# Optimization experiments

Hardware: AMD Instinct MI355X
Metric: run time of the kernel (lower is better)

The kernel has to match this reference:

```python
import jax, jax.numpy as jnp
import numpy as np

B, N, F = 32, 1024, 7
HID, HID_GLO, MLP_H, OUT = 256, 8, 64, 8
THRESHOLD = 0.3


def setup_inputs() -> dict:
    key = jax.random.key(0)
    ks = jax.random.split(key, 16)
    def lin(k, fan_out, fan_in):
        # xavier-uniform-like init
        lim = (6.0 / (fan_in + fan_out)) ** 0.5
        return jax.random.uniform(k, (fan_out, fan_in), jnp.float32, -lim, lim)
    return {
        "x": jax.random.normal(ks[0], (B, N, F), jnp.float32),
        "W1": lin(ks[1], HID, 2),   "b1": jnp.zeros((HID,), jnp.float32),
        "W2": lin(ks[2], HID, HID), "b2": jnp.zeros((HID,), jnp.float32),
        "Wfc": lin(ks[3], HID, HID), "bfc": jnp.zeros((HID,), jnp.float32),
        "Wg": lin(ks[4], HID_GLO, 2), "bg": jnp.zeros((HID_GLO,), jnp.float32),
        "Wm0": lin(ks[5], MLP_H, N * F), "bm0": jnp.zeros((MLP_H,), jnp.float32),
        "Wm1": lin(ks[6], MLP_H, MLP_H), "bm1": jnp.zeros((MLP_H,), jnp.float32),
        "Wp": lin(ks[7], OUT, MLP_H + HID + HID_GLO), "bp": jnp.zeros((OUT,), jnp.float32),
    }


def reference(x, W1, b1, W2, b2, Wfc, bfc, Wg, bg, Wm0, bm0, Wm1, bm1, Wp, bp):
    # --- GCN branch (torch code detaches node features & adjacency) ---
    pts = jax.lax.stop_gradient(x[:, :, 1:3])                     # [B,N,2]
    diff = pts[:, :, None, :] - pts[:, None, :, :]                # [B,N,N,2]
    dist = jnp.sqrt(jnp.sum(diff * diff, axis=-1))                # [B,N,N]
    adj = (dist < THRESHOLD).astype(x.dtype)                      # [B,N,N]
    dinv = 1.0 / jnp.sqrt(jnp.sum(adj, axis=-1))                  # [B,N] (>=1, self-loop)
    nadj = dinv[:, :, None] * adj * dinv[:, None, :]              # D^-1/2 A D^-1/2
    h = jax.nn.relu(jnp.einsum('bij,bjd->bid', nadj, pts) @ W1.T + b1)   # [B,N,256]
    g = jnp.einsum('bij,bjh->bih', nadj, h) @ W2.T + b2                  # [B,N,256]
    gcn_en = jnp.mean(g, axis=1) @ Wfc.T + bfc                    # [B,256]

    # --- global branch (torch code uses .item() -> constants) ---
    v = jax.lax.stop_gradient(x[:, :, 1:5])                       # [B,N,4]
    avg_speed = jnp.mean(jnp.linalg.norm(v[:, :, 2:4], axis=-1), axis=1)  # [B]
    density = 1.0 / jnp.max(dist, axis=(1, 2))                    # [B] (v3 == pts)
    glo_in = jnp.stack([avg_speed, density], axis=-1)             # [B,2]
    glo_en = jax.nn.relu(glo_in @ Wg.T + bg)                      # [B,8]

    # --- MLP branch on flattened x ---
    xf = x.reshape(x.shape[0], -1)                                # [B, N*F]
    xf = jax.nn.relu(xf @ Wm0.T + bm0)
    xf = jax.nn.relu(xf @ Wm1.T + bm1)                            # [B,64]

    out = jnp.concatenate([xf, gcn_en, glo_en], axis=1) @ Wp.T + bp  # [B,8]
    return out
```

## Files before the change

### kernel.cpp

```cpp
#include <hip/hip_runtime.h>

#define BB 32
#define NN 1024
#define FF 7
#define HID 256
#define MLPH 64
#define OUTN 8
#define CATN (MLPH + HID + 8)

__device__ __forceinline__ float wave_sum(float v) {
#pragma unroll
    for (int m = 32; m >= 1; m >>= 1) v += __shfl_xor(v, m, 64);
    return v;
}
__device__ __forceinline__ float wave_max(float v) {
#pragma unroll
    for (int m = 32; m >= 1; m >>= 1) v = fmaxf(v, __shfl_xor(v, m, 64));
    return v;
}

__global__ __launch_bounds__(256) void kA(const float* __restrict__ x,
                                          const float* __restrict__ Wm0,
                                          const float* __restrict__ bm0,
                                          const float* __restrict__ W2,
                                          const float* __restrict__ b2,
                                          const float* __restrict__ Wfc,
                                          const float* __restrict__ bfc,
                                          const float* __restrict__ Wp,
                                          float* __restrict__ degp,
                                          float* __restrict__ bmax,
                                          float* __restrict__ sumsp,
                                          float* __restrict__ xf1,
                                          float* __restrict__ E,
                                          float* __restrict__ cE) {
    __shared__ __align__(16) float l0[256];
    __shared__ __align__(16) float l1[256];
    __shared__ float red[256];
    __shared__ float wred[4];
    int tid  = threadIdx.x;
    int lane = tid & 63;
    int w    = tid >> 6;
    if (blockIdx.x < 2048) {
        int blk = blockIdx.x;
        int b  = blk >> 6;
        int jg = (blk >> 2) & 15;
        int ks = blk & 3;
        const float* xb = x + b * (NN * FF);
        int n = ks * 256 + tid;
        l0[tid] = xb[n * FF + 1];
        l1[tid] = xb[n * FF + 2];
        int j = jg * 64 + lane;
        float pj0 = xb[j * FF + 1];
        float pj1 = xb[j * FF + 2];
        __syncthreads();
        const float4* v0p = (const float4*)&l0[w * 64];
        const float4* v1p = (const float4*)&l1[w * 64];
        unsigned degv = 0u;
        float mx = 0.f;
#pragma unroll 4
        for (int g = 0; g < 16; ++g) {
            float4 v0 = v0p[g], v1 = v1p[g];
            float dxa = pj0 - v0.x, dya = pj1 - v1.x;
            float dxb = pj0 - v0.y, dyb = pj1 - v1.y;
            float dxc = pj0 - v0.z, dyc = pj1 - v1.z;
            float dxd = pj0 - v0.w, dyd = pj1 - v1.w;
            float da = fmaf(dya, dya, dxa * dxa);
            float db = fmaf(dyb, dyb, dxb * dxb);
            float dc = fmaf(dyc, dyc, dxc * dxc);
            float dd = fmaf(dyd, dyd, dxd * dxd);
            degv += (da <= 0.09f);
            degv += (db <= 0.09f);
            degv += (dc <= 0.09f);
            degv += (dd <= 0.09f);
            mx = fmaxf(fmaxf(mx, fmaxf(da, db)), fmaxf(dc, dd));
        }
        red[tid] = (float)degv;
        __syncthreads();
        if (tid < 64) {
            degp[ks * (BB * NN) + b * NN + jg * 64 + tid] =
                red[tid] + red[tid + 64] + red[tid + 128] + red[tid + 192];
        }
        mx = wave_max(mx);
        if (lane == 0) wred[w] = mx;
        __syncthreads();
        if (tid == 0)
            bmax[b * 64 + jg * 4 + ks] =
                fmaxf(fmaxf(wred[0], wred[1]), fmaxf(wred[2], wred[3]));
        if (jg == 0 && ks == 0) {
            float sp = 0.f;
            for (int nn = tid; nn < NN; nn += 256) {
                float vx = xb[nn * FF + 3], vy = xb[nn * FF + 4];
                sp += sqrtf(vx * vx + vy * vy);
            }
            sp = wave_sum(sp);
            __syncthreads();
            if (lane == 0) wred[w] = sp;
            __syncthreads();
            if (tid == 0) sumsp[b] = wred[0] + wred[1] + wred[2] + wred[3];
        }
    } else if (blockIdx.x < 2560) {
        int blk = blockIdx.x - 2048;
        int b  = blk >> 4;
        int hq = blk & 15;
        int h = hq * 4 + w;
        const float4* wrow = (const float4*)(Wm0 + h * (NN * FF));
        const float4* xrow = (const float4*)(x + b * (NN * FF));
        float4 a4 = {0.f, 0.f, 0.f, 0.f};
#pragma unroll 7
        for (int it = 0; it < 28; ++it) {
            float4 wv = wrow[it * 64 + lane];
            float4 xv = xrow[it * 64 + lane];
            a4.x = fmaf(wv.x, xv.x, a4.x);
            a4.y = fmaf(wv.y, xv.y, a4.y);
            a4.z = fmaf(wv.z, xv.z, a4.z);
            a4.w = fmaf(wv.w, xv.w, a4.w);
        }
        float s = (a4.x + a4.y) + (a4.z + a4.w);
        s = wave_sum(s);
        if (lane == 0) xf1[b * MLPH + h] = fmaxf(s + bm0[h], 0.f);
    } else {
        int o = blockIdx.x - 2560;
        l0[tid] = Wp[o * CATN + MLPH + tid];
        __syncthreads();
        float a = 0.f;
#pragma unroll 8
        for (int m = 0; m < HID; ++m) a = fmaf(l0[m], Wfc[m * HID + tid], a);
        l1[tid] = a;
        red[tid] = l0[tid] * bfc[tid];
        __syncthreads();
        float e = 0.f;
#pragma unroll 8
        for (int k = 0; k < HID; ++k) e = fmaf(l1[k], W2[k * HID + tid], e);
        E[o * HID + tid] = e;
        float c = fmaf(l1[tid], b2[tid], red[tid]);
        c = wave_sum(c);
        if (lane == 0) wred[w] = c;
        __syncthreads();
        if (tid == 0) cE[o] = wred[0] + wred[1] + wred[2] + wred[3];
    }
}

__global__ __launch_bounds__(256) void kB(const float* __restrict__ x,
                                          const float* __restrict__ degp,
                                          float* __restrict__ q0p,
                                          float* __restrict__ q1p,
                                          float* __restrict__ wjp) {
    __shared__ __align__(16) float l0[256];
    __shared__ __align__(16) float l1[256];
    __shared__ __align__(16) float di[256];
    __shared__ float r0[256], r1[256], r2[256];
    int blk = blockIdx.x;
    int b  = blk >> 6;
    int jg = (blk >> 2) & 15;
    int ks = blk & 3;
    int tid  = threadIdx.x;
    int lane = tid & 63;
    int w    = tid >> 6;
    const float* xb = x + b * (NN * FF);
    int n = ks * 256 + tid;
    l0[tid] = xb[n * FF + 1];
    l1[tid] = xb[n * FF + 2];
    {
        int o = b * NN + n;
        float d = degp[o] + degp[BB * NN + o] + degp[2 * BB * NN + o] + degp[3 * BB * NN + o];
        di[tid] = 1.0f / sqrtf(d);
    }
    int j = jg * 64 + lane;
    float pj0 = xb[j * FF + 1];
    float pj1 = xb[j * FF + 2];
    __syncthreads();
    const float4* v0p = (const float4*)&l0[w * 64];
    const float4* v1p = (const float4*)&l1[w * 64];
    const float4* vdp = (const float4*)&di[w * 64];
    float a0 = 0.f, a1 = 0.f, as = 0.f;
#pragma unroll 4
    for (int g = 0; g < 16; ++g) {
        float4 v0 = v0p[g], v1 = v1p[g], vd = vdp[g];
        float dxa = pj0 - v0.x, dya = pj1 - v1.x;
        float dxb = pj0 - v0.y, dyb = pj1 - v1.y;
        float dxc = pj0 - v0.z, dyc = pj1 - v1.z;
        float dxd = pj0 - v0.w, dyd = pj1 - v1.w;
        float da = fmaf(dya, dya, dxa * dxa);
        float db = fmaf(dyb, dyb, dxb * dxb);
        float dc = fmaf(dyc, dyc, dxc * dxc);
        float dd = fmaf(dyd, dyd, dxd * dxd);
        float ta = (da <= 0.09f) ? vd.x : 0.0f;
        float tb = (db <= 0.09f) ? vd.y : 0.0f;
        float tc = (dc <= 0.09f) ? vd.z : 0.0f;
        float td = (dd <= 0.09f) ? vd.w : 0.0f;
        a0 = fmaf(ta, v0.x, a0); a1 = fmaf(ta, v1.x, a1); as += ta;
        a0 = fmaf(tb, v0.y, a0); a1 = fmaf(tb, v1.y, a1); as += tb;
        a0 = fmaf(tc, v0.z, a0); a1 = fmaf(tc, v1.z, a1); as += tc;
        a0 = fmaf(td, v0.w, a0); a1 = fmaf(td, v1.w, a1); as += td;
    }
    r0[tid] = a0; r1[tid] = a1; r2[tid] = as;
    __syncthreads();
    if (tid < 64) {
        int jj = jg * 64 + tid;
        int o = b * NN + jj;
        float d = degp[o] + degp[BB * NN + o] + degp[2 * BB * NN + o] + degp[3 * BB * NN + o];
        float dj = 1.0f / sqrtf(d);
        float s0 = r0[tid] + r0[tid + 64] + r0[tid + 128] + r0[tid + 192];
        float s1 = r1[tid] + r1[tid + 64] + r1[tid + 128] + r1[tid + 192];
        float ss = r2[tid] + r2[tid + 64] + r2[tid + 128] + r2[tid + 192];
        int oo = ks * (BB * NN) + b * NN + jj;
        q0p[oo] = dj * s0;
        q1p[oo] = dj * s1;
        wjp[oo] = dj * ss * (1.0f / NN);
    }
}

__global__ __launch_bounds__(1024) void kF(const float* __restrict__ q0p,
                                           const float* __restrict__ q1p,
                                           const float* __restrict__ wjp,
                                           const float* __restrict__ W1,
                                           const float* __restrict__ b1,
                                           const float* __restrict__ Wg,
                                           const float* __restrict__ bg,
                                           const float* __restrict__ Wm1,
                                           const float* __restrict__ bm1,
                                           const float* __restrict__ Wp,
                                           const float* __restrict__ bp,
                                           const float* __restrict__ xf1,
                                           const float* __restrict__ bmax,
                                           const float* __restrict__ sumsp,
                                           const float* __restrict__ E,
                                           const float* __restrict__ cE,
                                           float* __restrict__ out) {
    __shared__ __align__(16) float sq0[NN];
    __shared__ __align__(16) float sq1[NN];
    __shared__ __align__(16) float sw[NN];
    __shared__ __align__(16) float hp[4][HID];
    __shared__ __align__(16) float hs[HID];
    __shared__ float sx1[MLPH];
    __shared__ float sxf2[MLPH];
    __shared__ float sglo[8];
    __shared__ float smax;
    int b = blockIdx.x;
    int tid = threadIdx.x;
    {
        int o = b * NN + tid;
        sq0[tid] = q0p[o] + q0p[BB * NN + o] + q0p[2 * BB * NN + o] + q0p[3 * BB * NN + o];
        sq1[tid] = q1p[o] + q1p[BB * NN + o] + q1p[2 * BB * NN + o] + q1p[3 * BB * NN + o];
        sw[tid]  = wjp[o] + wjp[BB * NN + o] + wjp[2 * BB * NN + o] + wjp[3 * BB * NN + o];
    }
    if (tid >= 384 && tid < 448) {
        float v = bmax[b * 64 + (tid - 384)];
        v = wave_max(v);
        if (tid == 384) smax = v;
    }
    if (tid >= 448 && tid < 512) sx1[tid - 448] = xf1[b * MLPH + (tid - 448)];
    __syncthreads();
    {
        int h  = tid & 255;
        int jq = tid >> 8;
        float w10 = W1[h * 2], w11 = W1[h * 2 + 1], bb = b1[h];
        float acc = 0.f;
        const float4* q0v4 = (const float4*)&sq0[jq * 256];
        const float4* q1v4 = (const float4*)&sq1[jq * 256];
        const float4* wv4  = (const float4*)&sw[jq * 256];
#pragma unroll 4
        for (int g = 0; g < 64; ++g) {
            float4 q0v = q0v4[g], q1v = q1v4[g], wv = wv4[g];
            acc = fmaf(wv.x, fmaxf(fmaf(q1v.x, w11, fmaf(q0v.x, w10, bb)), 0.f), acc);
            acc = fmaf(wv.y, fmaxf(fmaf(q1v.y, w11, fmaf(q0v.y, w10, bb)), 0.f), acc);
            acc = fmaf(wv.z, fmaxf(fmaf(q1v.z, w11, fmaf(q0v.z, w10, bb)), 0.f), acc);
            acc = fmaf(wv.w, fmaxf(fmaf(q1v.w, w11, fmaf(q0v.w, w10, bb)), 0.f), acc);
        }
        hp[jq][h] = acc;
    }
    __syncthreads();
    if (tid < HID) {
        hs[tid] = hp[0][tid] + hp[1][tid] + hp[2][tid] + hp[3][tid];
    } else if (tid < HID + MLPH) {
        int t = tid - HID;
        float a = bm1[t];
        const float* wv = Wm1 + t * MLPH;
#pragma unroll
        for (int k = 0; k < MLPH; ++k) a = fmaf(wv[k], sx1[k], a);
        sxf2[t] = fmaxf(a, 0.f);
    } else if (tid < HID + MLPH + 8) {
        int t = tid - HID - MLPH;
        float avg  = sumsp[b] * (1.0f / NN);
        float dens = 1.0f / sqrtf(smax);
        sglo[t] = fmaxf(fmaf(Wg[t * 2], avg, fmaf(Wg[t * 2 + 1], dens, bg[t])), 0.f);
    }
    __syncthreads();
    if (tid < 512) {
        int o = tid >> 6, lane = tid & 63;
        const float* Eo = E + o * HID;
        float a = Eo[lane] * hs[lane];
        a = fmaf(Eo[lane + 64],  hs[lane + 64],  a);
        a = fmaf(Eo[lane + 128], hs[lane + 128], a);
        a = fmaf(Eo[lane + 192], hs[lane + 192], a);
        a = fmaf(Wp[o * CATN + lane], sxf2[lane], a);
        a = wave_sum(a);
        if (lane == 0) {
            const float* wg = Wp + o * CATN + MLPH + HID;
#pragma unroll
            for (int g = 0; g < 8; ++g) a = fmaf(wg[g], sglo[g], a);
            out[b * OUTN + o] = a + cE[o] + bp[o];
        }
    }
}

extern "C" void kernel_launch(void* const* d_in, const int* in_sizes, int n_in,
                              void* d_out, int out_size, void* d_ws, size_t ws_size,
                              hipStream_t stream) {
    const float* x   = (const float*)d_in[0];
    const float* W1  = (const float*)d_in[1];
    const float* b1  = (const float*)d_in[2];
    const float* W2  = (const float*)d_in[3];
    const float* b2  = (const float*)d_in[4];
    const float* Wfc = (const float*)d_in[5];
    const float* bfc = (const float*)d_in[6];
    const float* Wg  = (const float*)d_in[7];
    const float* bg  = (const float*)d_in[8];
    const float* Wm0 = (const float*)d_in[9];
    const float* bm0 = (const float*)d_in[10];
    const float* Wm1 = (const float*)d_in[11];
    const float* bm1 = (const float*)d_in[12];
    const float* Wp  = (const float*)d_in[13];
    const float* bp  = (const float*)d_in[14];
    float* out = (float*)d_out;
    float* ws = (float*)d_ws;

    float* degp  = ws;
    float* q0p   = ws + 131072;
    float* q1p   = ws + 262144;
    float* wjp   = ws + 393216;
    float* bmax  = ws + 524288;
    float* sumsp = ws + 526336;
    float* xf1   = ws + 526368;
    float* E     = ws + 528416;
    float* cE    = ws + 530464;

    kA<<<2568,    256,  0, stream>>>(x, Wm0, bm0, W2, b2, Wfc, bfc, Wp,
                                     degp, bmax, sumsp, xf1, E, cE);
    kB<<<BB * 64, 256,  0, stream>>>(x, degp, q0p, q1p, wjp);
    kF<<<BB,      1024, 0, stream>>>(q0p, q1p, wjp, W1, b1, Wg, bg,
                                     Wm1, bm1, Wp, bp,
                                     xf1, bmax, sumsp, E, cE, out);
}
```

Baseline: 129.9 us.

## Fuse three-kernel pipeline into single cooperative persistent kernel with grid syncs

Replaces the kA/kB/kF launches with one cooperative kernel of 512 persistent blocks that loop over work units and separate stages with grid.sync(). The Wm0 GEMV is split into partial chunks interleaved with the degree pass. The final per-batch hidden reduction is spread across 128 blocks instead of 32 large blocks, and point data is loaded through coalesced float4 staging into shared memory. The aim is to remove launch gaps and the serial 32-block tail, at the cost of grid-barrier overhead and extra workspace traffic for partial results.

```diff
diff --git a/kernel.cpp b/kernel.cpp
--- a/kernel.cpp
+++ b/kernel.cpp
@@ -1,4 +1,7 @@
 #include <hip/hip_runtime.h>
+#include <hip/hip_cooperative_groups.h>
+
+namespace cg = cooperative_groups;
 
 #define BB 32
 #define NN 1024
@@ -17,6 +20,287 @@
 #pragma unroll
     for (int m = 32; m >= 1; m >>= 1) v = fmaxf(v, __shfl_xor(v, m, 64));
     return v;
+}
+
+__global__ __launch_bounds__(256, 4) void kAll(
+    const float* __restrict__ x,
+    const float* __restrict__ W1,  const float* __restrict__ b1,
+    const float* __restrict__ W2,  const float* __restrict__ b2,
+    const float* __restrict__ Wfc, const float* __restrict__ bfc,
+    const float* __restrict__ Wg,  const float* __restrict__ bg,
+    const float* __restrict__ Wm0, const float* __restrict__ bm0,
+    const float* __restrict__ Wm1, const float* __restrict__ bm1,
+    const float* __restrict__ Wp,  const float* __restrict__ bp,
+    float* ws, float* __restrict__ out) {
+    __shared__ __align__(16) float sx[1792];
+    __shared__ __align__(16) float s0[256];
+    __shared__ __align__(16) float s1[256];
+    __shared__ __align__(16) float s2[256];
+    __shared__ __align__(16) float s3[256];
+    __shared__ __align__(16) float s4[256];
+    __shared__ __align__(16) float s5[256];
+    __shared__ float wred[4];
+
+    float* degp  = ws;
+    float* q0p   = ws + 131072;
+    float* q1p   = ws + 262144;
+    float* wjp   = ws + 393216;
+    float* hp    = ws + 524288;
+    float* mlp_p = ws + 557056;
+    float* bmaxw = ws + 565248;
+    float* sumsp = ws + 567296;
+    float* xf2   = ws + 567328;
+    float* sglo  = ws + 569376;
+    float* E     = ws + 569632;
+    float* cE    = ws + 571680;
+
+    cg::grid_group grid = cg::this_grid();
+    int blk = blockIdx.x, tid = threadIdx.x, lane = tid & 63, w = tid >> 6;
+
+    for (int u = 0; u < 4; ++u) {
+        int unit = blk * 4 + u;
+        int b = unit >> 6, jg = (unit >> 2) & 15, ks = unit & 3;
+        const float* xb = x + b * (NN * FF);
+        {
+            const float4* xw4 = (const float4*)(xb + ks * 1792);
+            float4* sx4 = (float4*)sx;
+            sx4[tid] = xw4[tid];
+            if (tid < 192) sx4[256 + tid] = xw4[256 + tid];
+        }
+        int j = jg * 64 + lane;
+        float pj0 = xb[j * FF + 1];
+        float pj1 = xb[j * FF + 2];
+        __syncthreads();
+        s0[tid] = sx[tid * 7 + 1];
+        s1[tid] = sx[tid * 7 + 2];
+        __syncthreads();
+        const float4* v0p = (const float4*)&s0[w * 64];
+        const float4* v1p = (const float4*)&s1[w * 64];
+        unsigned degv = 0u;
+        float mx = 0.f;
+#pragma unroll 4
+        for (int g = 0; g < 16; ++g) {
+            float4 v0 = v0p[g], v1 = v1p[g];
+            float dxa = pj0 - v0.x, dya = pj1 - v1.x;
+            float dxb = pj0 - v0.y, dyb = pj1 - v1.y;
+            float dxc = pj0 - v0.z, dyc = pj1 - v1.z;
+            float dxd = pj0 - v0.w, dyd = pj1 - v1.w;
+            float da = fmaf(dya, dya, dxa * dxa);
+            float db = fmaf(dyb, dyb, dxb * dxb);
+            float dc = fmaf(dyc, dyc, dxc * dxc);
+            float dd = fmaf(dyd, dyd, dxd * dxd);
+            degv += (da <= 0.09f);
+            degv += (db <= 0.09f);
+            degv += (dc <= 0.09f);
+            degv += (dd <= 0.09f);
+            mx = fmaxf(fmaxf(mx, fmaxf(da, db)), fmaxf(dc, dd));
+        }
+        s2[tid] = (float)degv;
+        __syncthreads();
+        if (tid < 64) {
+            degp[ks * (BB * NN) + b * NN + jg * 64 + tid] =
+                s2[tid] + s2[tid + 64] + s2[tid + 128] + s2[tid + 192];
+        }
+        mx = wave_max(mx);
+        if (lane == 0) wred[w] = mx;
+        __syncthreads();
+        if (tid == 0)
+            bmaxw[b * 64 + jg * 4 + ks] =
+                fmaxf(fmaxf(wred[0], wred[1]), fmaxf(wred[2], wred[3]));
+        {
+            int id = unit * 4 + w;
+            int mb = id >> 8, mh = (id >> 2) & 63, mc = id & 3;
+            const float4* wr = (const float4*)(Wm0 + mh * (NN * FF) + mc * 1792);
+            const float4* xr = (const float4*)(x + mb * (NN * FF) + mc * 1792);
+            float4 a4 = {0.f, 0.f, 0.f, 0.f};
+#pragma unroll
+            for (int it = 0; it < 7; ++it) {
+                float4 wv = wr[it * 64 + lane];
+                float4 xv = xr[it * 64 + lane];
+                a4.x = fmaf(wv.x, xv.x, a4.x);
+                a4.y = fmaf(wv.y, xv.y, a4.y);
+                a4.z = fmaf(wv.z, xv.z, a4.z);
+                a4.w = fmaf(wv.w, xv.w, a4.w);
+            }
+            float s = (a4.x + a4.y) + (a4.z + a4.w);
+            s = wave_sum(s);
+            if (lane == 0) mlp_p[id] = s;
+        }
+        if (jg == 0 && ks == 0) {
+            float sp = 0.f;
+            for (int nn = tid; nn < NN; nn += 256) {
+                float vx = xb[nn * FF + 3], vy = xb[nn * FF + 4];
+                sp += sqrtf(vx * vx + vy * vy);
+            }
+            sp = wave_sum(sp);
+            __syncthreads();
+            if (lane == 0) wred[w] = sp;
+            __syncthreads();
+            if (tid == 0) sumsp[b] = wred[0] + wred[1] + wred[2] + wred[3];
+        }
+        __syncthreads();
+    }
+    grid.sync();
+    for (int u = 0; u < 4; ++u) {
+        int unit = blk * 4 + u;
+        int b = unit >> 6, jg = (unit >> 2) & 15, ks = unit & 3;
+        const float* xb = x + b * (NN * FF);
+        {
+            const float4* xw4 = (const float4*)(xb + ks * 1792);
+            float4* sx4 = (float4*)sx;
+            sx4[tid] = xw4[tid];
+            if (tid < 192) sx4[256 + tid] = xw4[256 + tid];
+        }
+        {
+            int o = b * NN + ks * 256 + tid;
+            float d = degp[o] + degp[BB * NN + o] + degp[2 * BB * NN + o]
+                    + degp[3 * BB * NN + o];
+            s2[tid] = 1.0f / sqrtf(d);
+        }
+        int j = jg * 64 + lane;
+        float pj0 = xb[j * FF + 1];
+        float pj1 = xb[j * FF + 2];
+        __syncthreads();
+        s0[tid] = sx[tid * 7 + 1];
+        s1[tid] = sx[tid * 7 + 2];
+        __syncthreads();
+        const float4* v0p = (const float4*)&s0[w * 64];
+        const float4* v1p = (const float4*)&s1[w * 64];
+        const float4* vdp = (const float4*)&s2[w * 64];
+        float a0 = 0.f, a1 = 0.f, as = 0.f;
+#pragma unroll 4
+        for (int g = 0; g < 16; ++g) {
+            float4 v0 = v0p[g], v1 = v1p[g], vd = vdp[g];
+            float dxa = pj0 - v0.x, dya = pj1 - v1.x;
+            float dxb = pj0 - v0.y, dyb = pj1 - v1.y;
+            float dxc = pj0 - v0.z, dyc = pj1 - v1.z;
+            float dxd = pj0 - v0.w, dyd = pj1 - v1.w;
+            float da = fmaf(dya, dya, dxa * dxa);
+            float db = fmaf(dyb, dyb, dxb * dxb);
+            float dc = fmaf(dyc, dyc, dxc * dxc);
+            float dd = fmaf(dyd, dyd, dxd * dxd);
+            float ta = (da <= 0.09f) ? vd.x : 0.0f;
+            float tb = (db <= 0.09f) ? vd.y : 0.0f;
+            float tc = (dc <= 0.09f) ? vd.z : 0.0f;
+            float td = (dd <= 0.09f) ? vd.w : 0.0f;
+            a0 = fmaf(ta, v0.x, a0); a1 = fmaf(ta, v1.x, a1); as += ta;
+            a0 = fmaf(tb, v0.y, a0); a1 = fmaf(tb, v1.y, a1); as += tb;
+            a0 = fmaf(tc, v0.z, a0); a1 = fmaf(tc, v1.z, a1); as += tc;
+            a0 = fmaf(td, v0.w, a0); a1 = fmaf(td, v1.w, a1); as += td;
+        }
+        s3[tid] = a0; s4[tid] = a1; s5[tid] = as;
+        __syncthreads();
+        if (tid < 64) {
+            int jj = jg * 64 + tid;
+            int o = b * NN + jj;
+            float d = degp[o] + degp[BB * NN + o] + degp[2 * BB * NN + o]
+                    + degp[3 * BB * NN + o];
+            float dj = 1.0f / sqrtf(d);
+            float q0v = s3[tid] + s3[tid + 64] + s3[tid + 128] + s3[tid + 192];
+            float q1v = s4[tid] + s4[tid + 64] + s4[tid + 128] + s4[tid + 192];
+            float ssv = s5[tid] + s5[tid + 64] + s5[tid + 128] + s5[tid + 192];
+            int oo = ks * (BB * NN) + b * NN + jj;
+            q0p[oo] = dj * q0v;
+            q1p[oo] = dj * q1v;
+            wjp[oo] = dj * ssv * (1.0f / NN);
+        }
+        __syncthreads();
+    }
+    grid.sync();
+    if (blk < 128) {
+        int b = blk >> 2, jq = blk & 3;
+        int o = b * NN + jq * 256 + tid;
+        s0[tid] = q0p[o] + q0p[BB * NN + o] + q0p[2 * BB * NN + o] + q0p[3 * BB * NN + o];
+        s1[tid] = q1p[o] + q1p[BB * NN + o] + q1p[2 * BB * NN + o] + q1p[3 * BB * NN + o];
+        s2[tid] = wjp[o] + wjp[BB * NN + o] + wjp[2 * BB * NN + o] + wjp[3 * BB * NN + o];
+        __syncthreads();
+        float w10 = W1[tid * 2], w11 = W1[tid * 2 + 1], bb = b1[tid];
+        float acc = 0.f;
+        const float4* q0v4 = (const float4*)s0;
+        const float4* q1v4 = (const float4*)s1;
+        const float4* wv4  = (const float4*)s2;
+#pragma unroll 4
+        for (int g = 0; g < 64; ++g) {
+            float4 q0v = q0v4[g], q1v = q1v4[g], wv = wv4[g];
+            acc = fmaf(wv.x, fmaxf(fmaf(q1v.x, w11, fmaf(q0v.x, w10, bb)), 0.f), acc);
+            acc = fmaf(wv.y, fmaxf(fmaf(q1v.y, w11, fmaf(q0v.y, w10, bb)), 0.f), acc);
+            acc = fmaf(wv.z, fmaxf(fmaf(q1v.z, w11, fmaf(q0v.z, w10, bb)), 0.f), acc);
+            acc = fmaf(wv.w, fmaxf(fmaf(q1v.w, w11, fmaf(q0v.w, w10, bb)), 0.f), acc);
+        }
+        hp[jq * (BB * HID) + b * HID + tid] = acc;
+    } else if (blk < 136) {
+        int b = (blk - 128) * 4 + (tid >> 6), h = lane;
+        float4 p = *(const float4*)&mlp_p[(b * 64 + h) * 4];
+        s0[tid] = fmaxf(((p.x + p.y) + (p.z + p.w)) + bm0[h], 0.f);
+        __syncthreads();
+        float a = bm1[h];
+        const float* wv = Wm1 + h * MLPH;
+        const float* xv = &s0[(tid >> 6) * 64];
+#pragma unroll
+        for (int k = 0; k < MLPH; ++k) a = fmaf(wv[k], xv[k], a);
+        xf2[b * 64 + h] = fmaxf(a, 0.f);
+    } else if (blk < 168) {
+        int b = blk - 136;
+        if (tid < 64) {
+            float v = bmaxw[b * 64 + tid];
+            v = wave_max(v);
+            if (tid < 8) {
+                float avg  = sumsp[b] * (1.0f / NN);
+                float dens = 1.0f / sqrtf(v);
+                sglo[b * 8 + tid] =
+                    fmaxf(fmaf(Wg[tid * 2], avg, fmaf(Wg[tid * 2 + 1], dens, bg[tid])), 0.f);
+            }
+        }
+    } else if (blk < 176) {
+        int o = blk - 168;
+        s0[tid] = Wp[o * CATN + MLPH + tid];
+        __syncthreads();
+        float a = 0.f;
+#pragma unroll 8
+        for (int m = 0; m < HID; ++m) a = fmaf(s0[m], Wfc[m * HID + tid], a);
+        s1[tid] = a;
+        s2[tid] = s0[tid] * bfc[tid];
+        __syncthreads();
+        float e = 0.f;
+#pragma unroll 8
+        for (int k = 0; k < HID; ++k) e = fmaf(s1[k], W2[k * HID + tid], e);
+        E[o * HID + tid] = e;
+        float c = fmaf(s1[tid], b2[tid], s2[tid]);
+        c = wave_sum(c);
+        if (lane == 0) wred[w] = c;
+        __syncthreads();
+        if (tid == 0) cE[o] = wred[0] + wred[1] + wred[2] + wred[3];
+    }
+    grid.sync();
+    if (blk < 32) {
+        int b = blk;
+        {
+            int o = b * HID + tid;
+            s0[tid] = hp[o] + hp[BB * HID + o] + hp[2 * BB * HID + o]
+                    + hp[3 * BB * HID + o];
+        }
+        if (tid < 64) s1[tid] = xf2[b * 64 + tid];
+        if (tid < 8)  s2[tid] = sglo[b * 8 + tid];
+        __syncthreads();
+        int oo = w;
+#pragma unroll
+        for (int rep = 0; rep < 2; ++rep) {
+            const float* Eo = E + oo * HID;
+            float a = Eo[lane] * s0[lane];
+            a = fmaf(Eo[lane + 64],  s0[lane + 64],  a);
+            a = fmaf(Eo[lane + 128], s0[lane + 128], a);
+            a = fmaf(Eo[lane + 192], s0[lane + 192], a);
+            a = fmaf(Wp[oo * CATN + lane], s1[lane], a);
+            a = wave_sum(a);
+            if (lane == 0) {
+                const float* wg = Wp + oo * CATN + MLPH + HID;
+#pragma unroll
+                for (int g = 0; g < 8; ++g) a = fmaf(wg[g], s2[g], a);
+                out[b * OUTN + oo] = a + cE[oo] + bp[oo];
+            }
+            oo += 4;
+        }
+    }
 }
 
 __global__ __launch_bounds__(256) void kA(const float* __restrict__ x,
@@ -37,14 +321,10 @@
     __shared__ __align__(16) float l1[256];
     __shared__ float red[256];
     __shared__ float wred[4];
-    int tid  = threadIdx.x;
-    int lane = tid & 63;
-    int w    = tid >> 6;
+    int tid = threadIdx.x, lane = tid & 63, w = tid >> 6;
     if (blockIdx.x < 2048) {
         int blk = blockIdx.x;
-        int b  = blk >> 6;
-        int jg = (blk >> 2) & 15;
-        int ks = blk & 3;
+        int b = blk >> 6, jg = (blk >> 2) & 15, ks = blk & 3;
         const float* xb = x + b * (NN * FF);
         int n = ks * 256 + tid;
         l0[tid] = xb[n * FF + 1];
@@ -100,8 +380,7 @@
         }
     } else if (blockIdx.x < 2560) {
         int blk = blockIdx.x - 2048;
-        int b  = blk >> 4;
-        int hq = blk & 15;
+        int b = blk >> 4, hq = blk & 15;
         int h = hq * 4 + w;
         const float4* wrow = (const float4*)(Wm0 + h * (NN * FF));
         const float4* xrow = (const float4*)(x + b * (NN * FF));
@@ -150,12 +429,8 @@
     __shared__ __align__(16) float di[256];
     __shared__ float r0[256], r1[256], r2[256];
     int blk = blockIdx.x;
-    int b  = blk >> 6;
-    int jg = (blk >> 2) & 15;
-    int ks = blk & 3;
-    int tid  = threadIdx.x;
-    int lane = tid & 63;
-    int w    = tid >> 6;
+    int b = blk >> 6, jg = (blk >> 2) & 15, ks = blk & 3;
+    int tid = threadIdx.x, lane = tid & 63, w = tid >> 6;
     const float* xb = x + b * (NN * FF);
     int n = ks * 256 + tid;
     l0[tid] = xb[n * FF + 1];
@@ -200,13 +475,13 @@
         int o = b * NN + jj;
         float d = degp[o] + degp[BB * NN + o] + degp[2 * BB * NN + o] + degp[3 * BB * NN + o];
         float dj = 1.0f / sqrtf(d);
-        float s0 = r0[tid] + r0[tid + 64] + r0[tid + 128] + r0[tid + 192];
-        float s1 = r1[tid] + r1[tid + 64] + r1[tid + 128] + r1[tid + 192];
-        float ss = r2[tid] + r2[tid + 64] + r2[tid + 128] + r2[tid + 192];
+        float s0v = r0[tid] + r0[tid + 64] + r0[tid + 128] + r0[tid + 192];
+        float s1v = r1[tid] + r1[tid + 64] + r1[tid + 128] + r1[tid + 192];
+        float ssv = r2[tid] + r2[tid + 64] + r2[tid + 128] + r2[tid + 192];
         int oo = ks * (BB * NN) + b * NN + jj;
-        q0p[oo] = dj * s0;
-        q1p[oo] = dj * s1;
-        wjp[oo] = dj * ss * (1.0f / NN);
+        q0p[oo] = dj * s0v;
+        q1p[oo] = dj * s1v;
+        wjp[oo] = dj * ssv * (1.0f / NN);
     }
 }
 
@@ -230,14 +505,13 @@
     __shared__ __align__(16) float sq0[NN];
     __shared__ __align__(16) float sq1[NN];
     __shared__ __align__(16) float sw[NN];
-    __shared__ __align__(16) float hp[4][HID];
+    __shared__ __align__(16) float hpp[4][HID];
     __shared__ __align__(16) float hs[HID];
     __shared__ float sx1[MLPH];
     __shared__ float sxf2[MLPH];
     __shared__ float sglo[8];
     __shared__ float smax;
-    int b = blockIdx.x;
-    int tid = threadIdx.x;
+    int b = blockIdx.x, tid = threadIdx.x;
     {
         int o = b * NN + tid;
         sq0[tid] = q0p[o] + q0p[BB * NN + o] + q0p[2 * BB * NN + o] + q0p[3 * BB * NN + o];
@@ -252,8 +526,7 @@
     if (tid >= 448 && tid < 512) sx1[tid - 448] = xf1[b * MLPH + (tid - 448)];
     __syncthreads();
     {
-        int h  = tid & 255;
-        int jq = tid >> 8;
+        int h = tid & 255, jq = tid >> 8;
         float w10 = W1[h * 2], w11 = W1[h * 2 + 1], bb = b1[h];
         float acc = 0.f;
         const float4* q0v4 = (const float4*)&sq0[jq * 256];
@@ -267,11 +540,11 @@
             acc = fmaf(wv.z, fmaxf(fmaf(q1v.z, w11, fmaf(q0v.z, w10, bb)), 0.f), acc);
             acc = fmaf(wv.w, fmaxf(fmaf(q1v.w, w11, fmaf(q0v.w, w10, bb)), 0.f), acc);
         }
-        hp[jq][h] = acc;
+        hpp[jq][h] = acc;
     }
     __syncthreads();
     if (tid < HID) {
-        hs[tid] = hp[0][tid] + hp[1][tid] + hp[2][tid] + hp[3][tid];
+        hs[tid] = hpp[0][tid] + hpp[1][tid] + hpp[2][tid] + hpp[3][tid];
     } else if (tid < HID + MLPH) {
         int t = tid - HID;
         float a = bm1[t];
@@ -323,8 +596,27 @@
     const float* Wp  = (const float*)d_in[13];
     const float* bp  = (const float*)d_in[14];
     float* out = (float*)d_out;
-    float* ws = (float*)d_ws;
-
+    float* ws  = (float*)d_ws;
+
+    int nb = 0;
+    hipError_t qe = hipOccupancyMaxActiveBlocksPerMultiprocessor(
+        &nb, reinterpret_cast<const void*>(&kAll), 256, 0);
+    if (qe == hipSuccess && nb >= 2) {
+        void* args[] = {
+            (void*)&x,
+            (void*)&W1,  (void*)&b1,
+            (void*)&W2,  (void*)&b2,
+            (void*)&Wfc, (void*)&bfc,
+            (void*)&Wg,  (void*)&bg,
+            (void*)&Wm0, (void*)&bm0,
+            (void*)&Wm1, (void*)&bm1,
+            (void*)&Wp,  (void*)&bp,
+            (void*)&ws,  (void*)&out,
+        };
+        hipError_t le = hipLaunchCooperativeKernel((void*)kAll, dim3(512), dim3(256),
+                                                   args, 0, stream);
+        if (le == hipSuccess) return;
+    }
     float* degp  = ws;
     float* q0p   = ws + 131072;
     float* q1p   = ws + 262144;
@@ -334,7 +626,6 @@
     float* xf1   = ws + 526368;
     float* E     = ws + 528416;
     float* cE    = ws + 530464;
-
     kA<<<2568,    256,  0, stream>>>(x, Wm0, bm0, W2, b2, Wfc, bfc, Wp,
                                      degp, bmax, sumsp, xf1, E, cE);
     kB<<<BB * 64, 256,  0, stream>>>(x, degp, q0p, q1p, wjp);
```

Result: slower. 309.5 us (+138.3%).

## Use 1024-thread blocks covering all nodes, removing partial-degree splits and merging MLP work

Applied to the files above, without the earlier changes.

Restructures the pairwise-distance kernels so each 1024-thread block covers all N source nodes for a 64-node target group. This removes the 4-way k-split partial buffers and their cross-block summation of degree, q0, q1 and wj. The first MLP layer's dot products are folded into the same blocks as per-quarter partials, which the final kernel reduces and biases. Workspace traffic and block count shrink, at the cost of larger blocks, more shared memory per block, and less scheduling granularity (520 and 512 blocks).

```diff
diff --git a/kernel.cpp b/kernel.cpp
--- a/kernel.cpp
+++ b/kernel.cpp
@@ -19,40 +19,32 @@
     return v;
 }
 
-__global__ __launch_bounds__(256) void kA(const float* __restrict__ x,
-                                          const float* __restrict__ Wm0,
-                                          const float* __restrict__ bm0,
-                                          const float* __restrict__ W2,
-                                          const float* __restrict__ b2,
-                                          const float* __restrict__ Wfc,
-                                          const float* __restrict__ bfc,
-                                          const float* __restrict__ Wp,
-                                          float* __restrict__ degp,
-                                          float* __restrict__ bmax,
-                                          float* __restrict__ sumsp,
-                                          float* __restrict__ xf1,
-                                          float* __restrict__ E,
-                                          float* __restrict__ cE) {
-    __shared__ __align__(16) float l0[256];
-    __shared__ __align__(16) float l1[256];
-    __shared__ float red[256];
-    __shared__ float wred[4];
-    int tid  = threadIdx.x;
-    int lane = tid & 63;
-    int w    = tid >> 6;
-    if (blockIdx.x < 2048) {
-        int blk = blockIdx.x;
-        int b  = blk >> 6;
-        int jg = (blk >> 2) & 15;
-        int ks = blk & 3;
+__global__ __launch_bounds__(1024, 8) void kA(const float* __restrict__ x,
+                                              const float* __restrict__ Wm0,
+                                              const float* __restrict__ W2,
+                                              const float* __restrict__ b2,
+                                              const float* __restrict__ Wfc,
+                                              const float* __restrict__ bfc,
+                                              const float* __restrict__ Wp,
+                                              float* __restrict__ deg,
+                                              float* __restrict__ bmaxp,
+                                              float* __restrict__ spd,
+                                              float* __restrict__ mlp_p,
+                                              float* __restrict__ E,
+                                              float* __restrict__ cE) {
+    __shared__ __align__(16) float l0[NN];
+    __shared__ __align__(16) float l1[NN];
+    __shared__ __align__(16) float red[NN];
+    __shared__ float wred[16];
+    int blk = blockIdx.x, tid = threadIdx.x, lane = tid & 63, w = tid >> 6;
+    if (blk < 512) {
+        int b = blk >> 4, jg = blk & 15;
         const float* xb = x + b * (NN * FF);
-        int n = ks * 256 + tid;
-        l0[tid] = xb[n * FF + 1];
-        l1[tid] = xb[n * FF + 2];
+        l0[tid] = xb[tid * FF + 1];
+        l1[tid] = xb[tid * FF + 2];
+        __syncthreads();
         int j = jg * 64 + lane;
-        float pj0 = xb[j * FF + 1];
-        float pj1 = xb[j * FF + 2];
-        __syncthreads();
+        float pj0 = l0[j], pj1 = l1[j];
         const float4* v0p = (const float4*)&l0[w * 64];
         const float4* v1p = (const float4*)&l1[w * 64];
         unsigned degv = 0u;
@@ -75,100 +67,93 @@
             mx = fmaxf(fmaxf(mx, fmaxf(da, db)), fmaxf(dc, dd));
         }
         red[tid] = (float)degv;
-        __syncthreads();
-        if (tid < 64) {
-            degp[ks * (BB * NN) + b * NN + jg * 64 + tid] =
-                red[tid] + red[tid + 64] + red[tid + 128] + red[tid + 192];
-        }
         mx = wave_max(mx);
         if (lane == 0) wred[w] = mx;
         __syncthreads();
-        if (tid == 0)
-            bmax[b * 64 + jg * 4 + ks] =
-                fmaxf(fmaxf(wred[0], wred[1]), fmaxf(wred[2], wred[3]));
-        if (jg == 0 && ks == 0) {
-            float sp = 0.f;
-            for (int nn = tid; nn < NN; nn += 256) {
-                float vx = xb[nn * FF + 3], vy = xb[nn * FF + 4];
-                sp += sqrtf(vx * vx + vy * vy);
+        if (tid < 64) {
+            float s = 0.f;
+#pragma unroll
+            for (int kk = 0; kk < 16; ++kk) s += red[kk * 64 + tid];
+            deg[b * NN + jg * 64 + tid] = s;
+        }
+        if (tid == 0) {
+            float m = wred[0];
+#pragma unroll
+            for (int i = 1; i < 16; ++i) m = fmaxf(m, wred[i]);
+            bmaxp[b * 16 + jg] = m;
+        }
+        if (w == 1) {
+            int n = jg * 64 + lane;
+            float vx = xb[n * FF + 3], vy = xb[n * FF + 4];
+            float sp = sqrtf(fmaf(vx, vx, vy * vy));
+            sp = wave_sum(sp);
+            if (lane == 0) spd[b * 16 + jg] = sp;
+        }
+        {
+            int id = blk * 16 + w;
+            int mb = id >> 8, mh = (id >> 2) & 63, mc = id & 3;
+            const float4* wr = (const float4*)(Wm0 + mh * (NN * FF) + mc * 1792);
+            const float4* xr = (const float4*)(x + mb * (NN * FF) + mc * 1792);
+            float4 a4 = {0.f, 0.f, 0.f, 0.f};
+#pragma unroll
+            for (int it = 0; it < 7; ++it) {
+                float4 wv = wr[it * 64 + lane];
+                float4 xv = xr[it * 64 + lane];
+                a4.x = fmaf(wv.x, xv.x, a4.x);
+                a4.y = fmaf(wv.y, xv.y, a4.y);
+                a4.z = fmaf(wv.z, xv.z, a4.z);
+                a4.w = fmaf(wv.w, xv.w, a4.w);
             }
-            sp = wave_sum(sp);
-            __syncthreads();
-            if (lane == 0) wred[w] = sp;
-            __syncthreads();
-            if (tid == 0) sumsp[b] = wred[0] + wred[1] + wred[2] + wred[3];
-        }
-    } else if (blockIdx.x < 2560) {
-        int blk = blockIdx.x - 2048;
-        int b  = blk >> 4;
-        int hq = blk & 15;
-        int h = hq * 4 + w;
-        const float4* wrow = (const float4*)(Wm0 + h * (NN * FF));
-        const float4* xrow = (const float4*)(x + b * (NN * FF));
-        float4 a4 = {0.f, 0.f, 0.f, 0.f};
-#pragma unroll 7
-        for (int it = 0; it < 28; ++it) {
-            float4 wv = wrow[it * 64 + lane];
-            float4 xv = xrow[it * 64 + lane];
-            a4.x = fmaf(wv.x, xv.x, a4.x);
-            a4.y = fmaf(wv.y, xv.y, a4.y);
-            a4.z = fmaf(wv.z, xv.z, a4.z);
-            a4.w = fmaf(wv.w, xv.w, a4.w);
-        }
-        float s = (a4.x + a4.y) + (a4.z + a4.w);
-        s = wave_sum(s);
-        if (lane == 0) xf1[b * MLPH + h] = fmaxf(s + bm0[h], 0.f);
+            float s = (a4.x + a4.y) + (a4.z + a4.w);
+            s = wave_sum(s);
+            if (lane == 0) mlp_p[id] = s;
+        }
     } else {
-        int o = blockIdx.x - 2560;
-        l0[tid] = Wp[o * CATN + MLPH + tid];
-        __syncthreads();
-        float a = 0.f;
+        int o = blk - 512;
+        if (tid < HID) l0[tid] = Wp[o * CATN + MLPH + tid];
+        __syncthreads();
+        if (tid < HID) {
+            float a = 0.f;
 #pragma unroll 8
-        for (int m = 0; m < HID; ++m) a = fmaf(l0[m], Wfc[m * HID + tid], a);
-        l1[tid] = a;
-        red[tid] = l0[tid] * bfc[tid];
-        __syncthreads();
-        float e = 0.f;
+            for (int m = 0; m < HID; ++m) a = fmaf(l0[m], Wfc[m * HID + tid], a);
+            l1[tid] = a;
+            red[tid] = l0[tid] * bfc[tid];
+        }
+        __syncthreads();
+        if (tid < HID) {
+            float e = 0.f;
 #pragma unroll 8
-        for (int k = 0; k < HID; ++k) e = fmaf(l1[k], W2[k * HID + tid], e);
-        E[o * HID + tid] = e;
-        float c = fmaf(l1[tid], b2[tid], red[tid]);
-        c = wave_sum(c);
-        if (lane == 0) wred[w] = c;
+            for (int k = 0; k < HID; ++k) e = fmaf(l1[k], W2[k * HID + tid], e);
+            E[o * HID + tid] = e;
+            float c = fmaf(l1[tid], b2[tid], red[tid]);
+            c = wave_sum(c);
+            if (lane == 0) wred[w] = c;
+        }
         __syncthreads();
         if (tid == 0) cE[o] = wred[0] + wred[1] + wred[2] + wred[3];
     }
 }
 
-__global__ __launch_bounds__(256) void kB(const float* __restrict__ x,
-                                          const float* __restrict__ degp,
-                                          float* __restrict__ q0p,
-                                          float* __restrict__ q1p,
-                                          float* __restrict__ wjp) {
-    __shared__ __align__(16) float l0[256];
-    __shared__ __align__(16) float l1[256];
-    __shared__ __align__(16) float di[256];
-    __shared__ float r0[256], r1[256], r2[256];
-    int blk = blockIdx.x;
-    int b  = blk >> 6;
-    int jg = (blk >> 2) & 15;
-    int ks = blk & 3;
-    int tid  = threadIdx.x;
-    int lane = tid & 63;
-    int w    = tid >> 6;
+__global__ __launch_bounds__(1024, 8) void kB(const float* __restrict__ x,
+                                              const float* __restrict__ deg,
+                                              float* __restrict__ q0,
+                                              float* __restrict__ q1,
+                                              float* __restrict__ wj) {
+    __shared__ __align__(16) float l0[NN];
+    __shared__ __align__(16) float l1[NN];
+    __shared__ __align__(16) float di[NN];
+    __shared__ __align__(16) float r0[NN];
+    __shared__ __align__(16) float r1[NN];
+    __shared__ __align__(16) float r2[NN];
+    int blk = blockIdx.x, tid = threadIdx.x, lane = tid & 63, w = tid >> 6;
+    int b = blk >> 4, jg = blk & 15;
     const float* xb = x + b * (NN * FF);
-    int n = ks * 256 + tid;
-    l0[tid] = xb[n * FF + 1];
-    l1[tid] = xb[n * FF + 2];
-    {
-        int o = b * NN + n;
-        float d = degp[o] + degp[BB * NN + o] + degp[2 * BB * NN + o] + degp[3 * BB * NN + o];
-        di[tid] = 1.0f / sqrtf(d);
-    }
+    l0[tid] = xb[tid * FF + 1];
+    l1[tid] = xb[tid * FF + 2];
+    di[tid] = 1.0f / sqrtf(deg[b * NN + tid]);
+    __syncthreads();
     int j = jg * 64 + lane;
-    float pj0 = xb[j * FF + 1];
-    float pj1 = xb[j * FF + 2];
-    __syncthreads();
+    float pj0 = l0[j], pj1 = l1[j];
     const float4* v0p = (const float4*)&l0[w * 64];
     const float4* v1p = (const float4*)&l1[w * 64];
     const float4* vdp = (const float4*)&di[w * 64];
@@ -196,64 +181,59 @@
     r0[tid] = a0; r1[tid] = a1; r2[tid] = as;
     __syncthreads();
     if (tid < 64) {
+        float s0 = 0.f, s1 = 0.f, ss = 0.f;
+#pragma unroll
+        for (int kk = 0; kk < 16; ++kk) {
+            s0 += r0[kk * 64 + tid];
+            s1 += r1[kk * 64 + tid];
+            ss += r2[kk * 64 + tid];
+        }
         int jj = jg * 64 + tid;
-        int o = b * NN + jj;
-        float d = degp[o] + degp[BB * NN + o] + degp[2 * BB * NN + o] + degp[3 * BB * NN + o];
-        float dj = 1.0f / sqrtf(d);
-        float s0 = r0[tid] + r0[tid + 64] + r0[tid + 128] + r0[tid + 192];
-        float s1 = r1[tid] + r1[tid + 64] + r1[tid + 128] + r1[tid + 192];
-        float ss = r2[tid] + r2[tid + 64] + r2[tid + 128] + r2[tid + 192];
-        int oo = ks * (BB * NN) + b * NN + jj;
-        q0p[oo] = dj * s0;
-        q1p[oo] = dj * s1;
-        wjp[oo] = dj * ss * (1.0f / NN);
-    }
-}
-
-__global__ __launch_bounds__(1024) void kF(const float* __restrict__ q0p,
-                                           const float* __restrict__ q1p,
-                                           const float* __restrict__ wjp,
-                                           const float* __restrict__ W1,
-                                           const float* __restrict__ b1,
-                                           const float* __restrict__ Wg,
-                                           const float* __restrict__ bg,
-                                           const float* __restrict__ Wm1,
-                                           const float* __restrict__ bm1,
-                                           const float* __restrict__ Wp,
-                                           const float* __restrict__ bp,
-                                           const float* __restrict__ xf1,
-                                           const float* __restrict__ bmax,
-                                           const float* __restrict__ sumsp,
-                                           const float* __restrict__ E,
-                                           const float* __restrict__ cE,
-                                           float* __restrict__ out) {
+        float dj = di[jj];
+        q0[b * NN + jj] = dj * s0;
+        q1[b * NN + jj] = dj * s1;
+        wj[b * NN + jj] = dj * ss * (1.0f / NN);
+    }
+}
+
+__global__ __launch_bounds__(1024, 4) void kF(const float* __restrict__ q0,
+                                              const float* __restrict__ q1,
+                                              const float* __restrict__ wj,
+                                              const float* __restrict__ W1,
+                                              const float* __restrict__ b1,
+                                              const float* __restrict__ Wg,
+                                              const float* __restrict__ bg,
+                                              const float* __restrict__ Wm1,
+                                              const float* __restrict__ bm1,
+                                              const float* __restrict__ Wp,
+                                              const float* __restrict__ bp,
+                                              const float* __restrict__ bm0,
+                                              const float* __restrict__ mlp_p,
+                                              const float* __restrict__ bmaxp,
+                                              const float* __restrict__ spd,
+                                              const float* __restrict__ E,
+                                              const float* __restrict__ cE,
+                                              float* __restrict__ out) {
     __shared__ __align__(16) float sq0[NN];
     __shared__ __align__(16) float sq1[NN];
     __shared__ __align__(16) float sw[NN];
-    __shared__ __align__(16) float hp[4][HID];
+    __shared__ __align__(16) float hpp[4][HID];
     __shared__ __align__(16) float hs[HID];
     __shared__ float sx1[MLPH];
     __shared__ float sxf2[MLPH];
     __shared__ float sglo[8];
-    __shared__ float smax;
-    int b = blockIdx.x;
-    int tid = threadIdx.x;
+    int b = blockIdx.x, tid = threadIdx.x;
+    sq0[tid] = q0[b * NN + tid];
+    sq1[tid] = q1[b * NN + tid];
+    sw[tid]  = wj[b * NN + tid];
+    if (tid >= 448 && tid < 512) {
+        int h = tid - 448;
+        float4 p = *(const float4*)&mlp_p[b * 256 + h * 4];
+        sx1[h] = fmaxf(((p.x + p.y) + (p.z + p.w)) + bm0[h], 0.f);
+    }
+    __syncthreads();
     {
-        int o = b * NN + tid;
-        sq0[tid] = q0p[o] + q0p[BB * NN + o] + q0p[2 * BB * NN + o] + q0p[3 * BB * NN + o];
-        sq1[tid] = q1p[o] + q1p[BB * NN + o] + q1p[2 * BB * NN + o] + q1p[3 * BB * NN + o];
-        sw[tid]  = wjp[o] + wjp[BB * NN + o] + wjp[2 * BB * NN + o] + wjp[3 * BB * NN + o];
-    }
-    if (tid >= 384 && tid < 448) {
-        float v = bmax[b * 64 + (tid - 384)];
-        v = wave_max(v);
-        if (tid == 384) smax = v;
-    }
-    if (tid >= 448 && tid < 512) sx1[tid - 448] = xf1[b * MLPH + (tid - 448)];
-    __syncthreads();
-    {
-        int h  = tid & 255;
-        int jq = tid >> 8;
+        int h = tid & 255, jq = tid >> 8;
         float w10 = W1[h * 2], w11 = W1[h * 2 + 1], bb = b1[h];
         float acc = 0.f;
         const float4* q0v4 = (const float4*)&sq0[jq * 256];
@@ -267,11 +247,11 @@
             acc = fmaf(wv.z, fmaxf(fmaf(q1v.z, w11, fmaf(q0v.z, w10, bb)), 0.f), acc);
             acc = fmaf(wv.w, fmaxf(fmaf(q1v.w, w11, fmaf(q0v.w, w10, bb)), 0.f), acc);
         }
-        hp[jq][h] = acc;
+        hpp[jq][h] = acc;
     }
     __syncthreads();
     if (tid < HID) {
-        hs[tid] = hp[0][tid] + hp[1][tid] + hp[2][tid] + hp[3][tid];
+        hs[tid] = hpp[0][tid] + hpp[1][tid] + hpp[2][tid] + hpp[3][tid];
     } else if (tid < HID + MLPH) {
         int t = tid - HID;
         float a = bm1[t];
@@ -281,8 +261,14 @@
         sxf2[t] = fmaxf(a, 0.f);
     } else if (tid < HID + MLPH + 8) {
         int t = tid - HID - MLPH;
-        float avg  = sumsp[b] * (1.0f / NN);
-        float dens = 1.0f / sqrtf(smax);
+        float mx = 0.f, sp = 0.f;
+#pragma unroll
+        for (int g = 0; g < 16; ++g) {
+            mx = fmaxf(mx, bmaxp[b * 16 + g]);
+            sp += spd[b * 16 + g];
+        }
+        float avg  = sp * (1.0f / NN);
+        float dens = 1.0f / sqrtf(mx);
         sglo[t] = fmaxf(fmaf(Wg[t * 2], avg, fmaf(Wg[t * 2 + 1], dens, bg[t])), 0.f);
     }
     __syncthreads();
@@ -323,22 +309,21 @@
     const float* Wp  = (const float*)d_in[13];
     const float* bp  = (const float*)d_in[14];
     float* out = (float*)d_out;
-    float* ws = (float*)d_ws;
-
-    float* degp  = ws;
-    float* q0p   = ws + 131072;
-    float* q1p   = ws + 262144;
-    float* wjp   = ws + 393216;
-    float* bmax  = ws + 524288;
-    float* sumsp = ws + 526336;
-    float* xf1   = ws + 526368;
-    float* E     = ws + 528416;
-    float* cE    = ws + 530464;
-
-    kA<<<2568,    256,  0, stream>>>(x, Wm0, bm0, W2, b2, Wfc, bfc, Wp,
-                                     degp, bmax, sumsp, xf1, E, cE);
-    kB<<<BB * 64, 256,  0, stream>>>(x, degp, q0p, q1p, wjp);
-    kF<<<BB,      1024, 0, stream>>>(q0p, q1p, wjp, W1, b1, Wg, bg,
-                                     Wm1, bm1, Wp, bp,
-                                     xf1, bmax, sumsp, E, cE, out);
-}
+    float* ws  = (float*)d_ws;
+
+    float* deg   = ws;
+    float* q0    = ws + 32768;
+    float* q1    = ws + 65536;
+    float* wj    = ws + 98304;
+    float* mlp_p = ws + 131072;
+    float* bmaxp = ws + 139264;
+    float* spd   = ws + 139776;
+    float* E     = ws + 140288;
+    float* cE    = ws + 142336;
+
+    kA<<<520, 1024, 0, stream>>>(x, Wm0, W2, b2, Wfc, bfc, Wp,
+                                 deg, bmaxp, spd, mlp_p, E, cE);
+    kB<<<512, 1024, 0, stream>>>(x, deg, q0, q1, wj);
+    kF<<<BB,  1024, 0, stream>>>(q0, q1, wj, W1, b1, Wg, bg, Wm1, bm1, Wp, bp,
+                                 bm0, mlp_p, bmaxp, spd, E, cE, out);
+}
```

Result: no change. 132.4 us (+2.0%).
